# Kernel tuning notes

Hardware: AMD Instinct MI355X
Metric: run time of the kernel (lower is better)

The kernel has to match this reference:

```python
import jax, jax.numpy as jnp
import numpy as np


def _cdist(a, b, p):
    # a: [B, N, D], b: [B, M, D] -> [B, N, M] pairwise Lp distance
    diff = jnp.abs(a[:, :, None, :] - b[:, None, :, :])  # [B, N, M, D]
    if p == 1:
        return jnp.sum(diff, axis=-1)
    return jnp.sum(diff ** p, axis=-1) ** (1.0 / p)


def setup_inputs() -> dict:
    key = jax.random.key(0)
    k1, k2, k3 = jax.random.split(key, 3)
    B, P, D = 32, 2048, 2
    pred = jax.random.normal(k1, (B, P, D), dtype=jnp.float32)
    gt = jax.random.normal(k2, (B, P, D), dtype=jnp.float32)
    gt_valid = jax.random.normal(k3, (B, P, D), dtype=jnp.float32)
    return {"pred": pred, "gt": gt, "gt_valid": gt_valid, "loss_type": 1}


def reference(pred, gt, gt_valid, loss_type):
    # matrix = cdist(pred, gt): [B, Np, Ng]; torch.min(dim=1) reduces over Np
    m1 = _cdist(pred, gt, loss_type)
    pred2gt_min = jnp.min(m1, axis=1)  # [B, Ng]
    # matrix = cdist(gt_valid, pred): [B, Ngv, Np]; min over dim=1 (Ngv)
    m2 = _cdist(gt_valid, pred, loss_type)
    gt2pred_min = jnp.min(m2, axis=1)  # [B, Np]
    return jnp.mean(jnp.stack([jnp.mean(pred2gt_min), jnp.mean(gt2pred_min)]))
```

## Files before the change

kernel.cpp:

```cpp
#include <hip/hip_runtime.h>


typedef float v2f __attribute__((ext_vector_type(2)));

#define BB 32
#define NN 2048
#define TPB 512
#define WAVES 8
#define TGT 128
#define CH (NN / WAVES)
#define NTILES (NN / TGT)
#define NBLK (2 * BB * NTILES)

__device__ __forceinline__ v2f pk_diff(v2f q_uniform, v2f negp) {
    v2f d;
    asm("v_pk_add_f32 %0, %1, %2" : "=v"(d) : "s"(q_uniform), "v"(negp));
    return d;
}

__global__ __launch_bounds__(TPB) void chamfer_l1_part(
    const float* __restrict__ pred,
    const float* __restrict__ gt,
    const float* __restrict__ gt_valid,
    float* __restrict__ bsum)
{
    const int bid  = blockIdx.x;
    const int dir  = bid >> 9;
    const int rem  = bid & 511;
    const int b    = rem >> 4;
    const int tile = rem & (NTILES - 1);
    const int lane = threadIdx.x & 63;
    const int wid  = __builtin_amdgcn_readfirstlane(threadIdx.x >> 6);

    const float* __restrict__ tgt = (dir == 0 ? gt   : pred)     + (size_t)b * NN * 2;
    const float* __restrict__ src = (dir == 0 ? pred : gt_valid) + (size_t)b * NN * 2
                                    + (size_t)wid * CH * 2;

    const int j0 = tile * TGT + lane;
    const int j1 = j0 + 64;

    v2f npA, npB;
    {
        float2 pA = reinterpret_cast<const float2*>(tgt)[j0];
        float2 pB = reinterpret_cast<const float2*>(tgt)[j1];
        npA = (v2f){-pA.x, -pA.y};
        npB = (v2f){-pB.x, -pB.y};
    }

    float a0 = 1e30f, a1 = 1e30f, b0 = 1e30f, b1 = 1e30f;
    const float4* __restrict__ srcv = reinterpret_cast<const float4*>(src);
    #pragma unroll 2
    for (int s = 0; s < CH / 2; s += 2) {
        float4 qa = srcv[s];
        float4 qb = srcv[s + 1];
        v2f q0 = (v2f){qa.x, qa.y};
        v2f q1 = (v2f){qa.z, qa.w};
        v2f q2 = (v2f){qb.x, qb.y};
        v2f q3 = (v2f){qb.z, qb.w};

        v2f dA0 = pk_diff(q0, npA), dA1 = pk_diff(q1, npA);
        v2f dA2 = pk_diff(q2, npA), dA3 = pk_diff(q3, npA);
        v2f dB0 = pk_diff(q0, npB), dB1 = pk_diff(q1, npB);
        v2f dB2 = pk_diff(q2, npB), dB3 = pk_diff(q3, npB);

        float sA0 = fabsf(dA0.x) + fabsf(dA0.y);
        float sA1 = fabsf(dA1.x) + fabsf(dA1.y);
        float sA2 = fabsf(dA2.x) + fabsf(dA2.y);
        float sA3 = fabsf(dA3.x) + fabsf(dA3.y);
        float sB0 = fabsf(dB0.x) + fabsf(dB0.y);
        float sB1 = fabsf(dB1.x) + fabsf(dB1.y);
        float sB2 = fabsf(dB2.x) + fabsf(dB2.y);
        float sB3 = fabsf(dB3.x) + fabsf(dB3.y);

        a0 = fminf(a0, fminf(sA0, sA1));
        a1 = fminf(a1, fminf(sA2, sA3));
        b0 = fminf(b0, fminf(sB0, sB1));
        b1 = fminf(b1, fminf(sB2, sB3));
    }
    const float mA = fminf(a0, a1);
    const float mB = fminf(b0, b1);

    __shared__ float part[WAVES][TGT];
    part[wid][lane]      = mA;
    part[wid][64 + lane] = mB;
    __syncthreads();

    __shared__ float wpart[2];
    if (threadIdx.x < 128) {
        const int t = threadIdx.x;
        float mm = part[0][t];
        #pragma unroll
        for (int w = 1; w < WAVES; ++w) mm = fminf(mm, part[w][t]);
        for (int off = 32; off > 0; off >>= 1)
            mm += __shfl_down(mm, off, 64);
        if ((t & 63) == 0) wpart[t >> 6] = mm;
    }
    __syncthreads();
    if (threadIdx.x == 0) bsum[bid] = wpart[0] + wpart[1];
}

__global__ __launch_bounds__(256) void chamfer_l1_reduce(
    const float* __restrict__ bsum,
    float* __restrict__ out)
{
    const int t = threadIdx.x;
    float4 v = reinterpret_cast<const float4*>(bsum)[t];
    float s = (v.x + v.y) + (v.z + v.w);
    for (int off = 32; off > 0; off >>= 1)
        s += __shfl_down(s, off, 64);
    __shared__ float w[4];
    if ((t & 63) == 0) w[t >> 6] = s;
    __syncthreads();
    if (t == 0)
        out[0] = (w[0] + w[1] + w[2] + w[3]) * (1.0f / (2.0f * BB * NN));
}

extern "C" void kernel_launch(void* const* d_in, const int* in_sizes, int n_in,
                              void* d_out, int out_size, void* d_ws, size_t ws_size,
                              hipStream_t stream) {
    const float* pred     = (const float*)d_in[0];
    const float* gt       = (const float*)d_in[1];
    const float* gt_valid = (const float*)d_in[2];
    float* out  = (float*)d_out;
    float* bsum = (float*)d_ws;

    chamfer_l1_part<<<NBLK, TPB, 0, stream>>>(pred, gt, gt_valid, bsum);
    chamfer_l1_reduce<<<1, 256, 0, stream>>>(bsum, out);
}
```

Measured before the change: 83.94 us.

## Stage source points in LDS and widen the unrolled min loop

Each block now copies the whole 2048-point source array for its batch into shared memory in one cooperative load. Each wave then reads its chunk back as LDS broadcast reads, where before it issued wave-uniform scalar global loads feeding hand-written packed-add assembly. The inner loop is unrolled to eight source points with four accumulators per target point, and plain vector subtraction replaces the inline v_pk_add_f32 asm. The aim is cheaper, better-overlapped source fetches and more instruction-level parallelism. The costs are a block barrier and 16 KB of LDS per block, and the source values now arrive in VGPRs instead of SGPR operands, so the compiler may not emit packed adds.

```diff
diff --git a/kernel.cpp b/kernel.cpp
--- a/kernel.cpp
+++ b/kernel.cpp
@@ -12,12 +12,6 @@
 #define NTILES (NN / TGT)
 #define NBLK (2 * BB * NTILES)
 
-__device__ __forceinline__ v2f pk_diff(v2f q_uniform, v2f negp) {
-    v2f d;
-    asm("v_pk_add_f32 %0, %1, %2" : "=v"(d) : "s"(q_uniform), "v"(negp));
-    return d;
-}
-
 __global__ __launch_bounds__(TPB) void chamfer_l1_part(
     const float* __restrict__ pred,
     const float* __restrict__ gt,
@@ -30,55 +24,70 @@
     const int b    = rem >> 4;
     const int tile = rem & (NTILES - 1);
     const int lane = threadIdx.x & 63;
-    const int wid  = __builtin_amdgcn_readfirstlane(threadIdx.x >> 6);
+    const int wid  = threadIdx.x >> 6;
 
     const float* __restrict__ tgt = (dir == 0 ? gt   : pred)     + (size_t)b * NN * 2;
-    const float* __restrict__ src = (dir == 0 ? pred : gt_valid) + (size_t)b * NN * 2
-                                    + (size_t)wid * CH * 2;
+    const float* __restrict__ src = (dir == 0 ? pred : gt_valid) + (size_t)b * NN * 2;
+
+    __shared__ v2f lds_src[NN];
+    {
+        const float4* gsrc = reinterpret_cast<const float4*>(src);
+        float4*       lsrc = reinterpret_cast<float4*>(lds_src);
+        lsrc[threadIdx.x]       = gsrc[threadIdx.x];
+        lsrc[threadIdx.x + TPB] = gsrc[threadIdx.x + TPB];
+    }
 
     const int j0 = tile * TGT + lane;
-    const int j1 = j0 + 64;
+    v2f pA, pB;
+    {
+        float2 tA = reinterpret_cast<const float2*>(tgt)[j0];
+        float2 tB = reinterpret_cast<const float2*>(tgt)[j0 + 64];
+        pA = (v2f){tA.x, tA.y};
+        pB = (v2f){tB.x, tB.y};
+    }
+    __syncthreads();
 
-    v2f npA, npB;
-    {
-        float2 pA = reinterpret_cast<const float2*>(tgt)[j0];
-        float2 pB = reinterpret_cast<const float2*>(tgt)[j1];
-        npA = (v2f){-pA.x, -pA.y};
-        npB = (v2f){-pB.x, -pB.y};
-    }
+    const v2f* __restrict__ ls = lds_src + wid * CH;
+    float a0 = 1e30f, a1 = 1e30f, a2 = 1e30f, a3 = 1e30f;
+    float b0 = 1e30f, b1 = 1e30f, b2 = 1e30f, b3 = 1e30f;
+    #pragma unroll 4
+    for (int s = 0; s < CH; s += 8) {
+        v2f q0 = ls[s+0], q1 = ls[s+1], q2 = ls[s+2], q3 = ls[s+3];
+        v2f q4 = ls[s+4], q5 = ls[s+5], q6 = ls[s+6], q7 = ls[s+7];
 
-    float a0 = 1e30f, a1 = 1e30f, b0 = 1e30f, b1 = 1e30f;
-    const float4* __restrict__ srcv = reinterpret_cast<const float4*>(src);
-    #pragma unroll 2
-    for (int s = 0; s < CH / 2; s += 2) {
-        float4 qa = srcv[s];
-        float4 qb = srcv[s + 1];
-        v2f q0 = (v2f){qa.x, qa.y};
-        v2f q1 = (v2f){qa.z, qa.w};
-        v2f q2 = (v2f){qb.x, qb.y};
-        v2f q3 = (v2f){qb.z, qb.w};
-
-        v2f dA0 = pk_diff(q0, npA), dA1 = pk_diff(q1, npA);
-        v2f dA2 = pk_diff(q2, npA), dA3 = pk_diff(q3, npA);
-        v2f dB0 = pk_diff(q0, npB), dB1 = pk_diff(q1, npB);
-        v2f dB2 = pk_diff(q2, npB), dB3 = pk_diff(q3, npB);
+        v2f dA0 = q0 - pA, dA1 = q1 - pA, dA2 = q2 - pA, dA3 = q3 - pA;
+        v2f dA4 = q4 - pA, dA5 = q5 - pA, dA6 = q6 - pA, dA7 = q7 - pA;
+        v2f dB0 = q0 - pB, dB1 = q1 - pB, dB2 = q2 - pB, dB3 = q3 - pB;
+        v2f dB4 = q4 - pB, dB5 = q5 - pB, dB6 = q6 - pB, dB7 = q7 - pB;
 
         float sA0 = fabsf(dA0.x) + fabsf(dA0.y);
         float sA1 = fabsf(dA1.x) + fabsf(dA1.y);
         float sA2 = fabsf(dA2.x) + fabsf(dA2.y);
         float sA3 = fabsf(dA3.x) + fabsf(dA3.y);
+        float sA4 = fabsf(dA4.x) + fabsf(dA4.y);
+        float sA5 = fabsf(dA5.x) + fabsf(dA5.y);
+        float sA6 = fabsf(dA6.x) + fabsf(dA6.y);
+        float sA7 = fabsf(dA7.x) + fabsf(dA7.y);
         float sB0 = fabsf(dB0.x) + fabsf(dB0.y);
         float sB1 = fabsf(dB1.x) + fabsf(dB1.y);
         float sB2 = fabsf(dB2.x) + fabsf(dB2.y);
         float sB3 = fabsf(dB3.x) + fabsf(dB3.y);
+        float sB4 = fabsf(dB4.x) + fabsf(dB4.y);
+        float sB5 = fabsf(dB5.x) + fabsf(dB5.y);
+        float sB6 = fabsf(dB6.x) + fabsf(dB6.y);
+        float sB7 = fabsf(dB7.x) + fabsf(dB7.y);
 
         a0 = fminf(a0, fminf(sA0, sA1));
         a1 = fminf(a1, fminf(sA2, sA3));
+        a2 = fminf(a2, fminf(sA4, sA5));
+        a3 = fminf(a3, fminf(sA6, sA7));
         b0 = fminf(b0, fminf(sB0, sB1));
         b1 = fminf(b1, fminf(sB2, sB3));
+        b2 = fminf(b2, fminf(sB4, sB5));
+        b3 = fminf(b3, fminf(sB6, sB7));
     }
-    const float mA = fminf(a0, a1);
-    const float mB = fminf(b0, b1);
+    const float mA = fminf(fminf(a0, a1), fminf(a2, a3));
+    const float mB = fminf(fminf(b0, b1), fminf(b2, b3));
 
     __shared__ float part[WAVES][TGT];
     part[wid][lane]      = mA;
```

New measurement: 80.31 us. -4.3%, faster.
